# Kernel tuning notes

Measured on AMD Instinct MI355X. Metric: run time of the kernel, lower is better.

## Reference

```python
import jax, jax.numpy as jnp
import numpy as np

DIM = 2048
HEADS = 16
DIM_HEAD = 128
FF_INNER = DIM * 4
SCALE_BASE = 512
EPS = 1e-5


def setup_inputs() -> dict:
    key = jax.random.key(0)
    k1, k2, k3, k4 = jax.random.split(key, 4)
    fused_out = HEADS * DIM_HEAD + DIM_HEAD + DIM_HEAD + 2 * FF_INNER  # 18688
    x = jax.random.normal(k1, (2, 2048, DIM), dtype=jnp.float32)
    gamma = jnp.ones((DIM,), dtype=jnp.float32)
    W_fused = jax.random.normal(k2, (DIM, fused_out), dtype=jnp.float32) * 0.02
    W_attn_out = jax.random.normal(k3, (HEADS * DIM_HEAD, DIM), dtype=jnp.float32) * 0.02
    W_ff_out = jax.random.normal(k4, (FF_INNER, DIM), dtype=jnp.float32) * 0.02
    return {"x": x, "gamma": gamma, "W_fused": W_fused, "W_attn_out": W_attn_out, "W_ff_out": W_ff_out}


def _rotate_half(t):
    t1, t2 = jnp.split(t, 2, axis=-1)
    return jnp.concatenate((-t2, t1), axis=-1)


def _rotary(n, dtype):
    # RotaryEmbedding with use_xpos=True, scale_base=512
    half = DIM_HEAD // 2
    inv_freq = 1.0 / (10000.0 ** (jnp.arange(0, DIM_HEAD, 2, dtype=dtype) / DIM_HEAD))
    t = jnp.arange(n, dtype=dtype)
    freqs = jnp.einsum('i,j->ij', t, inv_freq)          # [n, half]
    freqs = jnp.concatenate((freqs, freqs), axis=-1)    # [n, dh]
    scale_vec = (jnp.arange(0, DIM_HEAD, 2, dtype=dtype) + 0.4 * DIM_HEAD) / (1.4 * DIM_HEAD)
    power = (t - n // 2) / SCALE_BASE
    scale = scale_vec[None, :] ** power[:, None]        # [n, half]
    scale = jnp.concatenate((scale, scale), axis=-1)    # [n, dh]
    return freqs, scale


def _apply_rope(pos, t, scale):
    return t * jnp.cos(pos) * scale + _rotate_half(t) * jnp.sin(pos) * scale


def reference(x, gamma, W_fused, W_attn_out, W_ff_out):
    b, n, d = x.shape
    # LayerNorm (beta fixed at zero)
    mu = jnp.mean(x, axis=-1, keepdims=True)
    var = jnp.var(x, axis=-1, keepdims=True)
    xn = (x - mu) * jax.lax.rsqrt(var + EPS) * gamma

    proj = xn @ W_fused
    attn_inner = HEADS * DIM_HEAD
    q = proj[..., :attn_inner]
    k = proj[..., attn_inner:attn_inner + DIM_HEAD]
    v = proj[..., attn_inner + DIM_HEAD:attn_inner + 2 * DIM_HEAD]
    ff = proj[..., attn_inner + 2 * DIM_HEAD:]

    q = q.reshape(b, n, HEADS, DIM_HEAD).transpose(0, 2, 1, 3)  # b h n d

    pos, scale = _rotary(n, x.dtype)
    q = _apply_rope(pos, q, scale)            # broadcasts [n,dh] over b,h
    k = _apply_rope(pos, k, 1.0 / scale)      # k is [b, n, dh]

    # multi-query attention, causal
    sim = jnp.einsum('bhid,bjd->bhij', q, k) * (DIM_HEAD ** -0.5)
    causal_mask = jnp.triu(jnp.ones((n, n), dtype=bool), 1)
    sim = jnp.where(causal_mask, jnp.finfo(sim.dtype).min, sim)
    attn = jax.nn.softmax(sim, axis=-1)
    out = jnp.einsum('bhij,bjd->bhid', attn, v)
    out = out.transpose(0, 2, 1, 3).reshape(b, n, attn_inner)
    attn_out = out @ W_attn_out

    # SwiGLU: chunk -> silu(gate) * x
    ff_x, ff_gate = jnp.split(ff, 2, axis=-1)
    ff_out = (jax.nn.silu(ff_gate) * ff_x) @ W_ff_out

    return attn_out + ff_out
```

## Files before the change

kernel.cpp:

```cpp
#include <hip/hip_runtime.h>

typedef __attribute__((ext_vector_type(8))) short short8;
typedef __attribute__((ext_vector_type(4))) float floatx4;
typedef __attribute__((ext_vector_type(8))) unsigned short ushort8;
typedef __attribute__((ext_vector_type(2))) unsigned int uint2v;

#define FOUT 18688
#define FFI  8192
#define CATW 10240

__device__ __forceinline__ float b2f(unsigned short u){
  union { unsigned int i; float f; } v; v.i = ((unsigned int)u) << 16; return v.f;
}
__device__ __forceinline__ unsigned short f2b(float f){
  union { float f; unsigned int i; } v; v.f = f;
  unsigned int r = v.i + 0x7FFFu + ((v.i >> 16) & 1u);
  return (unsigned short)(r >> 16);
}
__device__ __forceinline__ void gld_lds16(const void* g, void* l){
  __builtin_amdgcn_global_load_lds((const __attribute__((address_space(1))) void*)g,
                                   (__attribute__((address_space(3))) void*)l, 16, 0, 0);
}

__global__ __launch_bounds__(256) void ln_kernel(const float* __restrict__ x,
                                                 const float* __restrict__ gamma,
                                                 unsigned short* __restrict__ xn){
  int row = blockIdx.x;
  const float* xr = x + (size_t)row * 2048;
  int tid = threadIdx.x;
  float v[8]; float s = 0.f, s2 = 0.f;
#pragma unroll
  for(int i=0;i<8;i++){ float t = xr[tid + i*256]; v[i]=t; s+=t; s2+=t*t; }
#pragma unroll
  for(int off=32; off>=1; off>>=1){ s += __shfl_down(s, off, 64); s2 += __shfl_down(s2, off, 64); }
  __shared__ float red[8];
  int wv = tid>>6, ln_ = tid&63;
  if(ln_==0){ red[wv] = s; red[wv+4] = s2; }
  __syncthreads();
  s  = red[0]+red[1]+red[2]+red[3];
  s2 = red[4]+red[5]+red[6]+red[7];
  float mu  = s * (1.f/2048.f);
  float var = s2 * (1.f/2048.f) - mu*mu;
  float rstd = rsqrtf(var + 1e-5f);
#pragma unroll
  for(int i=0;i<8;i++){
    float o = (v[i]-mu)*rstd*gamma[tid + i*256];
    xn[(size_t)row*2048 + tid + i*256] = f2b(o);
  }
}

__global__ void tcast_kernel(const float* __restrict__ W, unsigned short* __restrict__ Wt,
                             int R, int C, int S, int O){
  __shared__ float t[32][33];
  int bx = blockIdx.x*32, by = blockIdx.y*32;
  int tx = threadIdx.x, ty = threadIdx.y;
#pragma unroll
  for(int i=0;i<4;i++) t[ty+i*8][tx] = W[(size_t)(by+ty+i*8)*C + bx+tx];
  __syncthreads();
#pragma unroll
  for(int i=0;i<4;i++) Wt[(size_t)(bx+ty+i*8)*S + O + by+tx] = f2b(t[tx][ty+i*8]);
}

__global__ void vtrans_kernel(const unsigned short* __restrict__ proj, unsigned short* __restrict__ vt){
  __shared__ unsigned short t[32][33];
  int b = blockIdx.z;
  int n0 = blockIdx.x*32, d0 = blockIdx.y*32;
  int tx = threadIdx.x, ty = threadIdx.y;
#pragma unroll
  for(int i=0;i<4;i++) t[ty+i*8][tx] = proj[(size_t)(b*2048 + n0+ty+i*8)*FOUT + 2176 + d0+tx];
  __syncthreads();
#pragma unroll
  for(int i=0;i<4;i++) vt[((size_t)b*128 + d0+ty+i*8)*2048 + n0+tx] = t[tx][ty+i*8];
}

__global__ __launch_bounds__(256) void rope_tab_kernel(floatx4* __restrict__ tab){
  int idx = blockIdx.x*256 + threadIdx.x;
  int i = idx >> 6, j = idx & 63;
  float fj = (float)j, fi = (float)i;
  float p = fi * powf(10000.f, -fj*(1.f/64.f));
  float c = cosf(p), s = sinf(p);
  float sv = (2.f*fj + 51.2f) * (1.f/179.2f);
  float pw = (fi - 1024.f) * (1.f/512.f);
  float sc = powf(sv, pw);
  const float att = 0.08838834764831843f;
  floatx4 o; o[0]=c*sc*att; o[1]=s*sc*att; o[2]=c/sc; o[3]=s/sc;
  tab[idx] = o;
}

__global__ __launch_bounds__(256) void rope_kernel(unsigned short* __restrict__ proj,
                                                   const floatx4* __restrict__ tab){
  int row = blockIdx.x;
  int i = row & 2047;
  unsigned short* pr = proj + (size_t)row*FOUT;
  for(int item = threadIdx.x; item < 17*64; item += 256){
    int slot = item >> 6;
    int j = item & 63;
    floatx4 t = tab[i*64 + j];
    float cs = (slot==16) ? t[2] : t[0];
    float ss = (slot==16) ? t[3] : t[1];
    int colbase = (slot<16) ? slot*128 : 2048;
    float x1 = b2f(pr[colbase+j]);
    float x2 = b2f(pr[colbase+j+64]);
    pr[colbase+j]    = f2b(x1*cs - x2*ss);
    pr[colbase+j+64] = f2b(x2*cs + x1*ss);
  }
}

template<int MODE>
__global__ __launch_bounds__(512, 2) void gemm8p_kernel(const unsigned short* __restrict__ A,
                                                        const unsigned short* __restrict__ Bt,
                                                        unsigned short* __restrict__ Cb,
                                                        float* __restrict__ Cf,
                                                        int N, int K, int NT, int ntn,
                                                        size_t zstride){
  __shared__ unsigned short lds[65536];
  const int tid = threadIdx.x;
  const int wave = tid>>6, lane = tid&63;
  const int l15 = lane&15, l4 = lane>>4;
  const int wr = wave>>2, wc = wave&3;
  int id = blockIdx.x;
  int cpx = (int)gridDim.x >> 3;
  int swz = (id & 7)*cpx + (id >> 3);
  int tm = swz / ntn, tn = swz - tm*ntn;
  int kbase = (int)blockIdx.z * (NT*64);
  const unsigned short* Ab = A  + (size_t)tm*256*K + kbase;
  const unsigned short* Bb = Bt + (size_t)tn*256*K + kbase;
  if(MODE==1) Cf += (size_t)blockIdx.z * zstride;

  const int r0 = tid>>3;
  const int colc = ((tid&7) ^ (r0&7))*8;
  const int dstw = wave*512;

#define STAGE(t_, h_, isB_) do{ \
    const unsigned short* g_ = (isB_) ? Bb : Ab; \
    int db_ = (((t_)&1)<<15) + ((isB_)<<14) + ((h_)<<13) + dstw; \
    gld_lds16(g_ + (size_t)((h_)*128 + r0)*K + (t_)*64 + colc, &lds[db_]); \
    gld_lds16(g_ + (size_t)((h_)*128 + r0 + 64)*K + (t_)*64 + colc, &lds[db_ + 4096]); \
  }while(0)

  const int sw8 = l15&7;
  const int fo0 = ((l4    )^sw8)*8;
  const int fo1 = ((l4 + 4)^sw8)*8;
  const int albase = (wr*128 + l15)*64;
  const int blbase = 16384 + (wc*64 + l15)*64;

#define RD_A0(buf_, mf_, kk_) a0_[(mf_)*2+(kk_)] = *(const short8*)&lds[(buf_) + albase + (mf_)*1024 + ((kk_)?fo1:fo0)]
#define RD_A1(buf_, mf_, kk_) a1_[(mf_)*2+(kk_)] = *(const short8*)&lds[(buf_) + albase + 4096 + (mf_)*1024 + ((kk_)?fo1:fo0)]
#define RD_B(buf_, nf_, kk_)  b_[(nf_)*2+(kk_)]  = *(const short8*)&lds[(buf_) + blbase + (nf_)*1024 + ((kk_)?fo1:fo0)]
#define MFMA_Q(aarr_, mo_, no_) do{ \
  _Pragma("unroll") for(int kk=0; kk<2; kk++) \
  _Pragma("unroll") for(int mf=0; mf<4; mf++) \
  _Pragma("unroll") for(int nf=0; nf<2; nf++) \
    acc[(mo_)*4+mf][(no_)*2+nf] = __builtin_amdgcn_mfma_f32_16x16x32_bf16( \
      b_[((no_)*2+nf)*2+kk], aarr_[mf*2+kk], acc[(mo_)*4+mf][(no_)*2+nf], 0,0,0); \
}while(0)
#define LG0() do{ asm volatile("s_waitcnt lgkmcnt(0)" ::: "memory"); \
                  __builtin_amdgcn_sched_barrier(0); }while(0)

  floatx4 acc[8][4];
#pragma unroll
  for(int i=0;i<8;i++)
#pragma unroll
    for(int j=0;j<4;j++) acc[i][j] = (floatx4)0.f;

  short8 a0_[8], a1_[8], b_[8];

  STAGE(0,0,0); STAGE(0,1,0); STAGE(0,0,1); STAGE(0,1,1);
  STAGE(1,0,1); STAGE(1,1,1); STAGE(1,0,0);
  asm volatile("s_waitcnt vmcnt(6)" ::: "memory");
  __builtin_amdgcn_s_barrier();

  for(int t=0; t<NT; ++t){
    const int bufo = (t&1)<<15;
#pragma unroll
    for(int mf=0; mf<4; mf++){ RD_A0(bufo,mf,0); RD_A0(bufo,mf,1); }
    RD_B(bufo,0,0); RD_B(bufo,0,1); RD_B(bufo,1,0); RD_B(bufo,1,1);
    if(t+1 < NT) STAGE(t+1,1,0);
    asm volatile("s_waitcnt lgkmcnt(8)" ::: "memory");
    __builtin_amdgcn_s_barrier();
    LG0();
    __builtin_amdgcn_s_setprio(1);
    MFMA_Q(a0_,0,0);
    __builtin_amdgcn_s_setprio(0);
    __builtin_amdgcn_s_barrier();
    RD_B(bufo,2,0); RD_B(bufo,2,1); RD_B(bufo,3,0); RD_B(bufo,3,1);
    if(t+2 < NT) STAGE(t+2,0,1);
    __builtin_amdgcn_s_barrier();
    LG0();
    __builtin_amdgcn_s_setprio(1);
    MFMA_Q(a0_,0,1);
    __builtin_amdgcn_s_setprio(0);
    __builtin_amdgcn_s_barrier();
#pragma unroll
    for(int mf=0; mf<4; mf++){ RD_A1(bufo,mf,0); RD_A1(bufo,mf,1); }
    if(t+2 < NT) STAGE(t+2,1,1);
    __builtin_amdgcn_s_barrier();
    LG0();
    __builtin_amdgcn_s_setprio(1);
    MFMA_Q(a1_,1,0);
    __builtin_amdgcn_s_setprio(0);
    __builtin_amdgcn_s_barrier();
    if(t+2 < NT){
      STAGE(t+2,0,0);
      asm volatile("s_waitcnt vmcnt(6)" ::: "memory");
    } else if(t+1 < NT){
      asm volatile("s_waitcnt vmcnt(0)" ::: "memory");
    }
    __builtin_amdgcn_s_barrier();
    __builtin_amdgcn_s_setprio(1);
    MFMA_Q(a1_,1,1);
    __builtin_amdgcn_s_setprio(0);
    __builtin_amdgcn_s_barrier();
  }

  const size_t crow0 = (size_t)tm*256 + wr*128 + l15;
  const size_t ccol0 = (size_t)tn*256 + wc*64 + l4*4;
#pragma unroll
  for(int mi=0; mi<8; mi++){
    size_t row = crow0 + (mi>>2)*64 + (mi&3)*16;
#pragma unroll
    for(int nj=0; nj<4; nj++){
      size_t col = ccol0 + nj*16;
      floatx4 v = acc[mi][nj];
      if(MODE==0){
        uint2v u;
        u[0] = (unsigned int)f2b(v[0]) | ((unsigned int)f2b(v[1])<<16);
        u[1] = (unsigned int)f2b(v[2]) | ((unsigned int)f2b(v[3])<<16);
        *(uint2v*)&Cb[row*N + col] = u;
      } else {
        *(floatx4*)&Cf[row*N + col] = v;
      }
    }
  }
}

__global__ __launch_bounds__(256) void add2_kernel(const float* __restrict__ p0,
                                                   const float* __restrict__ p1,
                                                   float* __restrict__ o, int n4){
  for(int i = blockIdx.x*256 + threadIdx.x; i < n4; i += gridDim.x*256){
    floatx4 a = ((const floatx4*)p0)[i];
    floatx4 b = ((const floatx4*)p1)[i];
    ((floatx4*)o)[i] = a + b;
  }
}

__global__ __launch_bounds__(256) void attn_kernel(const unsigned short* __restrict__ proj,
                                                   const unsigned short* __restrict__ vt,
                                                   unsigned short* __restrict__ ao){
  __shared__ unsigned short lK[64*128];
  __shared__ unsigned short lV[128*64];
  __shared__ unsigned short lP[4*16*64];
  int qt = blockIdx.x, hh = blockIdx.y, b = blockIdx.z;
  int tid = threadIdx.x, wave = tid>>6, lane = tid&63;
  int l15 = lane&15, l4 = lane>>4;
  int q0 = qt*64;
  int qrow = q0 + wave*16 + l15;
  const unsigned short* qp = proj + (size_t)(b*2048 + qrow)*FOUT + hh*128 + l4*8;
  short8 qf[4];
#pragma unroll
  for(int ds=0; ds<4; ds++) qf[ds] = *(const short8*)(qp + ds*32);
  floatx4 po[8];
#pragma unroll
  for(int dt=0; dt<8; dt++) po[dt] = (floatx4)0.f;
  float mrun[4] = {-1e30f,-1e30f,-1e30f,-1e30f};
  float lrun[4] = {0.f,0.f,0.f,0.f};
  unsigned short* lPw = lP + wave*1024;
  const unsigned short* kb = proj + (size_t)(b*2048)*FOUT + 2048;
  const unsigned short* vb = vt + (size_t)b*128*2048;

  for(int kv=0; kv<=qt; kv++){
    int kv0 = kv*64;
#pragma unroll
    for(int it=0; it<4; it++){
      int f = it*256 + tid;
      int r = f>>4, pc = f&15;
      int gc = pc ^ (r&7);
      gld_lds16(kb + (size_t)(kv0 + r)*FOUT + gc*8, &lK[(it*256 + wave*64)*8]);
    }
#pragma unroll
    for(int it=0; it<4; it++){
      int f = it*256 + tid;
      int d = f>>3, pc = f&7;
      int gc = pc ^ (d&7);
      gld_lds16(vb + (size_t)d*2048 + kv0 + gc*8, &lV[(it*256 + wave*64)*8]);
    }
    __syncthreads();
    floatx4 sa[4];
#pragma unroll
    for(int jt=0;jt<4;jt++) sa[jt] = (floatx4)0.f;
#pragma unroll
    for(int jt=0;jt<4;jt++){
      int krow = jt*16 + l15;
#pragma unroll
      for(int ds=0; ds<4; ds++){
        int pc = (l4 + ds*4) ^ (krow&7);
        short8 kf = *(const short8*)&lK[krow*128 + pc*8];
        sa[jt] = __builtin_amdgcn_mfma_f32_16x16x32_bf16(qf[ds], kf, sa[jt], 0,0,0);
      }
    }
    float pv[4][4];
    bool diag = (kv == qt);
#pragma unroll
    for(int jt=0;jt<4;jt++){
#pragma unroll
      for(int r=0;r<4;r++){
        float s = sa[jt][r];
        if(diag && (kv0 + jt*16 + l15 > q0 + wave*16 + l4*4 + r)) s = -1e30f;
        pv[jt][r] = s;
      }
    }
    float mnew[4], corr[4];
#pragma unroll
    for(int r=0;r<4;r++){
      float mx = fmaxf(fmaxf(pv[0][r],pv[1][r]),fmaxf(pv[2][r],pv[3][r]));
      mx = fmaxf(mx, __shfl_xor(mx, 1, 64));
      mx = fmaxf(mx, __shfl_xor(mx, 2, 64));
      mx = fmaxf(mx, __shfl_xor(mx, 4, 64));
      mx = fmaxf(mx, __shfl_xor(mx, 8, 64));
      float mn = fmaxf(mrun[r], mx);
      corr[r] = __expf(mrun[r] - mn);
      mrun[r] = mn;
      mnew[r] = mn;
    }
    float rsum[4] = {0.f,0.f,0.f,0.f};
#pragma unroll
    for(int jt=0;jt<4;jt++){
#pragma unroll
      for(int r=0;r<4;r++){
        float p = __expf(pv[jt][r] - mnew[r]);
        pv[jt][r] = p;
        rsum[r] += p;
      }
    }
#pragma unroll
    for(int r=0;r<4;r++){
      float rs = rsum[r];
      rs += __shfl_xor(rs, 1, 64);
      rs += __shfl_xor(rs, 2, 64);
      rs += __shfl_xor(rs, 4, 64);
      rs += __shfl_xor(rs, 8, 64);
      lrun[r] = lrun[r]*corr[r] + rs;
    }
#pragma unroll
    for(int dt=0;dt<8;dt++){
#pragma unroll
      for(int r=0;r<4;r++) po[dt][r] *= corr[r];
    }
#pragma unroll
    for(int jt=0;jt<4;jt++){
#pragma unroll
      for(int r=0;r<4;r++){
        int i_ = l4*4 + r;
        int j = jt*16 + l15;
        int pc = (j>>3) ^ (i_&7);
        lPw[i_*64 + pc*8 + (j&7)] = f2b(pv[jt][r]);
      }
    }
    asm volatile("s_waitcnt lgkmcnt(0)" ::: "memory");
    short8 pf[2];
#pragma unroll
    for(int ks=0;ks<2;ks++){
      int pc = (l4 + ks*4) ^ (l15&7);
      pf[ks] = *(const short8*)&lPw[l15*64 + pc*8];
    }
#pragma unroll
    for(int dt=0;dt<8;dt++){
      int d = dt*16 + l15;
#pragma unroll
      for(int ks=0;ks<2;ks++){
        int pc = (ks*4 + l4) ^ (d&7);
        short8 vf = *(const short8*)&lV[d*64 + pc*8];
        po[dt] = __builtin_amdgcn_mfma_f32_16x16x32_bf16(pf[ks], vf, po[dt], 0,0,0);
      }
    }
    __syncthreads();
  }
#pragma unroll
  for(int r=0;r<4;r++){
    float inv = 1.f / lrun[r];
    size_t orow = (size_t)(b*2048 + q0 + wave*16 + l4*4 + r);
#pragma unroll
    for(int dt=0;dt<8;dt++){
      ao[orow*CATW + hh*128 + dt*16 + l15] = f2b(po[dt][r]*inv);
    }
  }
}

__global__ __launch_bounds__(256) void swiglu_kernel(const unsigned short* __restrict__ proj,
                                                     unsigned short* __restrict__ cat){
  size_t idx = (size_t)blockIdx.x*256 + threadIdx.x;
  int row = (int)(idx >> 10);
  int c8  = (int)(idx & 1023);
  const unsigned short* pr = proj + (size_t)row*FOUT + 2304 + c8*8;
  ushort8 xv = *(const ushort8*)pr;
  ushort8 gv = *(const ushort8*)(pr + FFI);
  ushort8 ov;
#pragma unroll
  for(int e=0;e<8;e++){
    float xf = b2f(xv[e]);
    float gf = b2f(gv[e]);
    float sg = gf / (1.f + __expf(-gf));
    ov[e] = f2b(sg*xf);
  }
  *(ushort8*)(cat + (size_t)row*CATW + 2048 + c8*8) = ov;
}

extern "C" void kernel_launch(void* const* d_in, const int* in_sizes, int n_in,
                              void* d_out, int out_size, void* d_ws, size_t ws_size,
                              hipStream_t stream){
  const float* x     = (const float*)d_in[0];
  const float* gamma = (const float*)d_in[1];
  const float* Wf    = (const float*)d_in[2];
  const float* Wa    = (const float*)d_in[3];
  const float* Wff   = (const float*)d_in[4];
  float* out = (float*)d_out;

  char* p = (char*)d_ws;
  unsigned short* xn    = (unsigned short*)p;  p += (size_t)4096*2048*2;
  unsigned short* WfT   = (unsigned short*)p;  p += (size_t)18688*2048*2;
  unsigned short* proj  = (unsigned short*)p;  p += (size_t)4096*18688*2;
  unsigned short* BtCat = (unsigned short*)p;  p += (size_t)2048*CATW*2;
  unsigned short* cat   = (unsigned short*)p;  p += (size_t)4096*CATW*2;
  unsigned short* vtb   = (unsigned short*)p;  p += (size_t)2*128*2048*2;
  floatx4*        rtab  = (floatx4*)p;         p += (size_t)2048*64*16;
  float* part = (float*)d_ws;

  ln_kernel<<<4096, 256, 0, stream>>>(x, gamma, xn);
  rope_tab_kernel<<<512, 256, 0, stream>>>(rtab);
  tcast_kernel<<<dim3(584,64),  dim3(32,8), 0, stream>>>(Wf,  WfT,   2048, 18688, 2048, 0);
  tcast_kernel<<<dim3(64,64),   dim3(32,8), 0, stream>>>(Wa,  BtCat, 2048, 2048,  CATW, 0);
  tcast_kernel<<<dim3(64,256),  dim3(32,8), 0, stream>>>(Wff, BtCat, 8192, 2048,  CATW, 2048);
  gemm8p_kernel<0><<<dim3(1168,1,1), 512, 0, stream>>>(xn, WfT, proj, nullptr, 18688, 2048, 32, 73, 0);
  rope_kernel<<<4096, 256, 0, stream>>>(proj, rtab);
  vtrans_kernel<<<dim3(64,4,2), dim3(32,8), 0, stream>>>(proj, vtb);
  attn_kernel<<<dim3(32,16,2), 256, 0, stream>>>(proj, vtb, cat);
  swiglu_kernel<<<16384, 256, 0, stream>>>(proj, cat);
  gemm8p_kernel<1><<<dim3(128,1,2), 512, 0, stream>>>(cat, BtCat, nullptr, part, 2048, 10240, 80, 8,
                                                      (size_t)4096*2048);
  add2_kernel<<<2048, 256, 0, stream>>>(part, part + (size_t)4096*2048, out, 2097152);
}
```

Baseline: 842.8 us.

## Rework GEMM to 4 waves with 128x128 per-wave tiles and prefetched fragments

Moves the bf16 GEMM from 8 waves of 512 threads to 4 waves of 256 threads, each owning a 128x128 output sub-tile (8x8 MFMA accumulators), so each LDS fragment read feeds more MFMAs. The k-loop is unrolled by two and ping-pongs B fragment registers, so the next tile's A/B fragments are loaded during the last MFMA quadrant. The aim is less LDS traffic per MFMA and fewer barrier stalls, at the cost of far higher register pressure (256 accumulator floats per lane), occupancy of one block per CU, and fewer threads issuing global-to-LDS copies.

New measurement: 1.279 ms. 51.7% more time.

```diff
diff --git a/kernel.cpp b/kernel.cpp
--- a/kernel.cpp
+++ b/kernel.cpp
@@ -106,8 +106,10 @@
   }
 }
 
+#define SCHED0() __builtin_amdgcn_sched_barrier(0)
+
 template<int MODE>
-__global__ __launch_bounds__(512, 2) void gemm8p_kernel(const unsigned short* __restrict__ A,
+__global__ __launch_bounds__(256, 1) void gemm4w_kernel(const unsigned short* __restrict__ A,
                                                         const unsigned short* __restrict__ Bt,
                                                         unsigned short* __restrict__ Cb,
                                                         float* __restrict__ Cf,
@@ -117,7 +119,7 @@
   const int tid = threadIdx.x;
   const int wave = tid>>6, lane = tid&63;
   const int l15 = lane&15, l4 = lane>>4;
-  const int wr = wave>>2, wc = wave&3;
+  const int wr = wave>>1, wc = wave&1;
   int id = blockIdx.x;
   int cpx = (int)gridDim.x >> 3;
   int swz = (id & 7)*cpx + (id >> 3);
@@ -131,95 +133,112 @@
   const int colc = ((tid&7) ^ (r0&7))*8;
   const int dstw = wave*512;
 
-#define STAGE(t_, h_, isB_) do{ \
+#define STG(t_, h_, isB_) do{ \
     const unsigned short* g_ = (isB_) ? Bb : Ab; \
-    int db_ = (((t_)&1)<<15) + ((isB_)<<14) + ((h_)<<13) + dstw; \
-    gld_lds16(g_ + (size_t)((h_)*128 + r0)*K + (t_)*64 + colc, &lds[db_]); \
-    gld_lds16(g_ + (size_t)((h_)*128 + r0 + 64)*K + (t_)*64 + colc, &lds[db_ + 4096]); \
+    int db_ = (((t_)&1)<<15) + ((isB_)*16384) + ((h_)*8192) + dstw; \
+    _Pragma("unroll") for(int s_=0; s_<4; s_++) \
+      gld_lds16(g_ + (size_t)((h_)*128 + s_*32 + r0)*K + (t_)*64 + colc, &lds[db_ + s_*2048]); \
   }while(0)
 
   const int sw8 = l15&7;
   const int fo0 = ((l4    )^sw8)*8;
   const int fo1 = ((l4 + 4)^sw8)*8;
   const int albase = (wr*128 + l15)*64;
-  const int blbase = 16384 + (wc*64 + l15)*64;
-
-#define RD_A0(buf_, mf_, kk_) a0_[(mf_)*2+(kk_)] = *(const short8*)&lds[(buf_) + albase + (mf_)*1024 + ((kk_)?fo1:fo0)]
-#define RD_A1(buf_, mf_, kk_) a1_[(mf_)*2+(kk_)] = *(const short8*)&lds[(buf_) + albase + 4096 + (mf_)*1024 + ((kk_)?fo1:fo0)]
-#define RD_B(buf_, nf_, kk_)  b_[(nf_)*2+(kk_)]  = *(const short8*)&lds[(buf_) + blbase + (nf_)*1024 + ((kk_)?fo1:fo0)]
-#define MFMA_Q(aarr_, mo_, no_) do{ \
+  const int blbase = 16384 + (wc*128 + l15)*64;
+
+#define RD_A(arr_, bufo_, mh_, mf_, kk_) arr_[(mf_)*2+(kk_)] = *(const short8*)&lds[(bufo_) + albase + (mh_)*4096 + (mf_)*1024 + ((kk_)?fo1:fo0)]
+#define RD_Bv(arr_, bufo_, nh_, nf_, kk_) arr_[(nf_)*2+(kk_)] = *(const short8*)&lds[(bufo_) + blbase + (nh_)*4096 + (nf_)*1024 + ((kk_)?fo1:fo0)]
+#define MFMA_Q(aarr_, barr_, mh_, nh_) do{ \
   _Pragma("unroll") for(int kk=0; kk<2; kk++) \
   _Pragma("unroll") for(int mf=0; mf<4; mf++) \
-  _Pragma("unroll") for(int nf=0; nf<2; nf++) \
-    acc[(mo_)*4+mf][(no_)*2+nf] = __builtin_amdgcn_mfma_f32_16x16x32_bf16( \
-      b_[((no_)*2+nf)*2+kk], aarr_[mf*2+kk], acc[(mo_)*4+mf][(no_)*2+nf], 0,0,0); \
+  _Pragma("unroll") for(int nf=0; nf<4; nf++) \
+    acc[(mh_)*4+mf][(nh_)*4+nf] = __builtin_amdgcn_mfma_f32_16x16x32_bf16( \
+      barr_[nf*2+kk], aarr_[mf*2+kk], acc[(mh_)*4+mf][(nh_)*4+nf], 0,0,0); \
 }while(0)
-#define LG0() do{ asm volatile("s_waitcnt lgkmcnt(0)" ::: "memory"); \
-                  __builtin_amdgcn_sched_barrier(0); }while(0)
-
-  floatx4 acc[8][4];
+
+  floatx4 acc[8][8];
 #pragma unroll
   for(int i=0;i<8;i++)
 #pragma unroll
-    for(int j=0;j<4;j++) acc[i][j] = (floatx4)0.f;
-
-  short8 a0_[8], a1_[8], b_[8];
-
-  STAGE(0,0,0); STAGE(0,1,0); STAGE(0,0,1); STAGE(0,1,1);
-  STAGE(1,0,1); STAGE(1,1,1); STAGE(1,0,0);
-  asm volatile("s_waitcnt vmcnt(6)" ::: "memory");
+    for(int j=0;j<8;j++) acc[i][j] = (floatx4)0.f;
+
+  short8 a0_[8], a1_[8], b0A_[8], b0B_[8], b1_[8];
+
+  STG(0,0,0); STG(0,1,0); STG(0,0,1); STG(0,1,1);
+  STG(1,0,1); STG(1,1,1); STG(1,0,0);
+  asm volatile("s_waitcnt vmcnt(12)" ::: "memory");
+  SCHED0();
   __builtin_amdgcn_s_barrier();
-
-  for(int t=0; t<NT; ++t){
-    const int bufo = (t&1)<<15;
-#pragma unroll
-    for(int mf=0; mf<4; mf++){ RD_A0(bufo,mf,0); RD_A0(bufo,mf,1); }
-    RD_B(bufo,0,0); RD_B(bufo,0,1); RD_B(bufo,1,0); RD_B(bufo,1,1);
-    if(t+1 < NT) STAGE(t+1,1,0);
-    asm volatile("s_waitcnt lgkmcnt(8)" ::: "memory");
-    __builtin_amdgcn_s_barrier();
-    LG0();
-    __builtin_amdgcn_s_setprio(1);
-    MFMA_Q(a0_,0,0);
-    __builtin_amdgcn_s_setprio(0);
-    __builtin_amdgcn_s_barrier();
-    RD_B(bufo,2,0); RD_B(bufo,2,1); RD_B(bufo,3,0); RD_B(bufo,3,1);
-    if(t+2 < NT) STAGE(t+2,0,1);
-    __builtin_amdgcn_s_barrier();
-    LG0();
-    __builtin_amdgcn_s_setprio(1);
-    MFMA_Q(a0_,0,1);
-    __builtin_amdgcn_s_setprio(0);
-    __builtin_amdgcn_s_barrier();
-#pragma unroll
-    for(int mf=0; mf<4; mf++){ RD_A1(bufo,mf,0); RD_A1(bufo,mf,1); }
-    if(t+2 < NT) STAGE(t+2,1,1);
-    __builtin_amdgcn_s_barrier();
-    LG0();
-    __builtin_amdgcn_s_setprio(1);
-    MFMA_Q(a1_,1,0);
-    __builtin_amdgcn_s_setprio(0);
-    __builtin_amdgcn_s_barrier();
-    if(t+2 < NT){
-      STAGE(t+2,0,0);
-      asm volatile("s_waitcnt vmcnt(6)" ::: "memory");
-    } else if(t+1 < NT){
-      asm volatile("s_waitcnt vmcnt(0)" ::: "memory");
-    }
-    __builtin_amdgcn_s_barrier();
-    __builtin_amdgcn_s_setprio(1);
-    MFMA_Q(a1_,1,1);
-    __builtin_amdgcn_s_setprio(0);
-    __builtin_amdgcn_s_barrier();
+  SCHED0();
+#pragma unroll
+  for(int mf=0; mf<4; mf++){ RD_A(a0_,0,0,mf,0); RD_A(a0_,0,0,mf,1); }
+#pragma unroll
+  for(int nf=0; nf<4; nf++){ RD_Bv(b0A_,0,0,nf,0); RD_Bv(b0A_,0,0,nf,1); }
+  SCHED0();
+
+#define KTILE(t_, BUFO, NBUFO, B0C, B0N) do{ \
+     \
+    _Pragma("unroll") for(int nf=0; nf<4; nf++){ RD_Bv(b1_,BUFO,1,nf,0); RD_Bv(b1_,BUFO,1,nf,1); } \
+    if((t_)+1 < NT) STG((t_)+1,1,0); \
+    __builtin_amdgcn_s_barrier(); \
+    asm volatile("s_waitcnt lgkmcnt(8)" ::: "memory"); \
+    SCHED0(); \
+    __builtin_amdgcn_s_setprio(1); \
+    MFMA_Q(a0_, B0C, 0, 0); \
+    __builtin_amdgcn_s_setprio(0); \
+    __builtin_amdgcn_s_barrier(); \
+     \
+    _Pragma("unroll") for(int mf=0; mf<4; mf++){ RD_A(a1_,BUFO,1,mf,0); RD_A(a1_,BUFO,1,mf,1); } \
+    if((t_)+2 < NT) STG((t_)+2,0,1); \
+    __builtin_amdgcn_s_barrier(); \
+    asm volatile("s_waitcnt lgkmcnt(8)" ::: "memory"); \
+    SCHED0(); \
+    __builtin_amdgcn_s_setprio(1); \
+    MFMA_Q(a0_, b1_, 0, 1); \
+    __builtin_amdgcn_s_setprio(0); \
+    __builtin_amdgcn_s_barrier(); \
+     \
+    if((t_)+2 < NT) STG((t_)+2,1,1); \
+    __builtin_amdgcn_s_barrier(); \
+    asm volatile("s_waitcnt lgkmcnt(0)" ::: "memory"); \
+    SCHED0(); \
+    __builtin_amdgcn_s_setprio(1); \
+    MFMA_Q(a1_, b1_, 1, 1); \
+    __builtin_amdgcn_s_setprio(0); \
+    __builtin_amdgcn_s_barrier(); \
+     \
+    if((t_)+2 < NT){ \
+      STG((t_)+2,0,0); \
+      asm volatile("s_waitcnt vmcnt(12)" ::: "memory"); \
+    } else if((t_)+1 < NT){ \
+      asm volatile("s_waitcnt vmcnt(0)" ::: "memory"); \
+    } \
+    SCHED0(); \
+    __builtin_amdgcn_s_barrier(); \
+    SCHED0(); \
+    __builtin_amdgcn_s_setprio(1); \
+    MFMA_Q(a1_, B0C, 1, 0); \
+    __builtin_amdgcn_s_setprio(0); \
+    if((t_)+1 < NT){ \
+      _Pragma("unroll") for(int mf=0; mf<4; mf++){ RD_A(a0_,NBUFO,0,mf,0); RD_A(a0_,NBUFO,0,mf,1); } \
+      _Pragma("unroll") for(int nf=0; nf<4; nf++){ RD_Bv(B0N,NBUFO,0,nf,0); RD_Bv(B0N,NBUFO,0,nf,1); } \
+    } \
+    SCHED0(); \
+    __builtin_amdgcn_s_barrier(); \
+  }while(0)
+
+  for(int t=0; t<NT; t+=2){
+    KTILE(t,   0,     32768, b0A_, b0B_);
+    KTILE(t+1, 32768, 0,     b0B_, b0A_);
   }
 
   const size_t crow0 = (size_t)tm*256 + wr*128 + l15;
-  const size_t ccol0 = (size_t)tn*256 + wc*64 + l4*4;
+  const size_t ccol0 = (size_t)tn*256 + wc*128 + l4*4;
 #pragma unroll
   for(int mi=0; mi<8; mi++){
-    size_t row = crow0 + (mi>>2)*64 + (mi&3)*16;
-#pragma unroll
-    for(int nj=0; nj<4; nj++){
+    size_t row = crow0 + mi*16;
+#pragma unroll
+    for(int nj=0; nj<8; nj++){
       size_t col = ccol0 + nj*16;
       floatx4 v = acc[mi][nj];
       if(MODE==0){
@@ -430,12 +449,12 @@
   tcast_kernel<<<dim3(584,64),  dim3(32,8), 0, stream>>>(Wf,  WfT,   2048, 18688, 2048, 0);
   tcast_kernel<<<dim3(64,64),   dim3(32,8), 0, stream>>>(Wa,  BtCat, 2048, 2048,  CATW, 0);
   tcast_kernel<<<dim3(64,256),  dim3(32,8), 0, stream>>>(Wff, BtCat, 8192, 2048,  CATW, 2048);
-  gemm8p_kernel<0><<<dim3(1168,1,1), 512, 0, stream>>>(xn, WfT, proj, nullptr, 18688, 2048, 32, 73, 0);
+  gemm4w_kernel<0><<<dim3(1168,1,1), 256, 0, stream>>>(xn, WfT, proj, nullptr, 18688, 2048, 32, 73, 0);
   rope_kernel<<<4096, 256, 0, stream>>>(proj, rtab);
   vtrans_kernel<<<dim3(64,4,2), dim3(32,8), 0, stream>>>(proj, vtb);
   attn_kernel<<<dim3(32,16,2), 256, 0, stream>>>(proj, vtb, cat);
   swiglu_kernel<<<16384, 256, 0, stream>>>(proj, cat);
-  gemm8p_kernel<1><<<dim3(128,1,2), 512, 0, stream>>>(cat, BtCat, nullptr, part, 2048, 10240, 80, 8,
+  gemm4w_kernel<1><<<dim3(128,1,2), 256, 0, stream>>>(cat, BtCat, nullptr, part, 2048, 10240, 80, 8,
                                                       (size_t)4096*2048);
   add2_kernel<<<2048, 256, 0, stream>>>(part, part + (size_t)4096*2048, out, 2097152);
 }
```
